# Kernel optimization log

Hardware: AMD Instinct MI355X
Metric: run time of the kernel (lower is better)

The kernel has to match this reference:

```python
import jax, jax.numpy as jnp
import numpy as np


def setup_inputs() -> dict:
    key = jax.random.key(0)
    ks = jax.random.split(key, 7)
    N = 262144
    Ka, La = 8, 8
    Kb, Lb, Mb = 8, 8, 4
    Kc, Lc, Mc = 8, 8, 4
    return {
        "x": jax.random.normal(ks[0], (N, 2), dtype=jnp.float32),
        "a_real": 0.001 * jax.random.normal(ks[1], (Ka, La), dtype=jnp.float32),
        "a_imag": 0.001 * jax.random.normal(ks[2], (Ka, La), dtype=jnp.float32),
        "b_real": 0.001 * jax.random.normal(ks[3], (Kb, Lb, Mb), dtype=jnp.float32),
        "b_imag": 0.001 * jax.random.normal(ks[4], (Kb, Lb, Mb), dtype=jnp.float32),
        "c_real": 0.001 * jax.random.normal(ks[5], (Kc, Lc, Mc), dtype=jnp.float32),
        "c_imag": 0.001 * jax.random.normal(ks[6], (Kc, Lc, Mc), dtype=jnp.float32),
    }


def _gmp(x, a_real, a_imag, b_real, b_imag, c_real, c_imag):
    # x: (N,2) real I/Q -> complex signal (iq_handler equivalent)
    xc = (x[:, 0] + 1j * x[:, 1]).astype(jnp.complex64)
    a = (a_real + 1j * a_imag).astype(jnp.complex64)   # (Ka,La)
    b = (b_real + 1j * b_imag).astype(jnp.complex64)   # (Kb,Lb,Mb)
    c = (c_real + 1j * c_imag).astype(jnp.complex64)   # (Kc,Lc,Mc)
    N = xc.shape[0]
    Ka, La = a.shape
    Kb, Lb, Mb = b.shape
    Kc, Lc, Mc = c.shape
    n = jnp.arange(N)

    # ---- aligned term (a): delayed taps, power series in |x[n-l]| ----
    idx_La = jnp.clip(n[None, :] - jnp.arange(La)[:, None], 0, N - 1)   # (La,N)
    x_La = xc[idx_La]                                                   # (La,N)
    pow_a = jnp.abs(x_La)[..., None] ** jnp.arange(Ka, dtype=jnp.float32)  # (La,N,Ka)
    term_a = jnp.einsum('kl,ln,lnk->n', a, x_La, pow_a)

    # ---- lagging cross-term (b): envelope delayed by extra m >= 0 ----
    idx_Lb = jnp.clip(n[None, :] - jnp.arange(Lb)[:, None], 0, N - 1)   # (Lb,N)
    x_Lb = xc[idx_Lb]                                                   # (Lb,N)
    idx_Mb = jnp.clip(n[None, None, :] - jnp.arange(Lb)[:, None, None]
                      - jnp.arange(Mb)[None, :, None], 0, N - 1)        # (Lb,Mb,N)
    x_Mb = xc[idx_Mb]                                                   # (Lb,Mb,N)
    pow_b = jnp.abs(x_Mb)[..., None] ** jnp.arange(Kb, dtype=jnp.float32)  # (Lb,Mb,N,Kb)
    term_b = jnp.einsum('klm,ln,lmnk->n', b, x_Lb, pow_b)

    # ---- leading cross-term (c): envelope advanced by m >= 0 ----
    idx_Lc = jnp.clip(n[None, :] - jnp.arange(Lc)[:, None], 0, N - 1)   # (Lc,N)
    x_Lc = xc[idx_Lc]                                                   # (Lc,N)
    idx_Mc = jnp.clip(n[None, None, :] - jnp.arange(Lc)[:, None, None]
                      + jnp.arange(Mc)[None, :, None], 0, N - 1)        # (Lc,Mc,N)
    x_Mc = xc[idx_Mc]                                                   # (Lc,Mc,N)
    pow_c = jnp.abs(x_Mc)[..., None] ** jnp.arange(Kc, dtype=jnp.float32)  # (Lc,Mc,N,Kc)
    term_c = jnp.einsum('klm,ln,lmnk->n', c, x_Lc, pow_c)

    y = term_a + term_b + term_c                                        # (N,) complex
    return jnp.stack([y.real, y.imag], axis=-1)                         # back to I/Q (N,2)


def reference(x, a_real, a_imag, b_real, b_imag, c_real, c_imag):
    return _gmp(x, a_real, a_imag, b_real, b_imag, c_real, c_imag)
```

## Files before the change

### kernel.cpp

```cpp
#include <hip/hip_runtime.h>
#include <type_traits>

typedef float v2f __attribute__((ext_vector_type(2)));

constexpr int BLOCK = 512;
constexpr int CHUNKS = 4;
constexpr int SPB = 256;
constexpr int SPBLK = SPB * CHUNKS;
constexpr int HALO_LO = 10;
constexpr int HALO_HI = 3;
constexpr int SIG = SPB + HALO_LO + HALO_HI;
constexpr int PSTRIDE = 128;

template<int I, int N, typename F>
__device__ __forceinline__ void unroll_for(F&& f) {
    if constexpr (I < N) {
        f(std::integral_constant<int, I>{});
        unroll_for<I + 1, N>(static_cast<F&&>(f));
    }
}

__global__ __launch_bounds__(BLOCK, 2) void gmp_kernel(
    const float* __restrict__ x,
    const float* __restrict__ a_re, const float* __restrict__ a_im,
    const float* __restrict__ b_re, const float* __restrict__ b_im,
    const float* __restrict__ c_re, const float* __restrict__ c_im,
    float* __restrict__ out, int N)
{
    __shared__ float sxr[SIG], sxi[SIG], sab[SIG];
    __shared__ __align__(16) float2 part[8][SPB];
    __shared__ __align__(16) float wlds[896];

    const int t = threadIdx.x;
    const int blk0 = blockIdx.x * SPBLK;
    const float2* x2 = (const float2*)x;

    if (t < SIG) {
        int g = blk0 - HALO_LO + t;
        g = max(0, min(N - 1, g));
        float2 v = x2[g];
        sxr[t] = v.x;
        sxi[t] = v.y;
        sab[t] = __builtin_amdgcn_sqrtf(fmaf(v.x, v.x, v.y * v.y));
    }

    if (t < 448) {
        int idx = t;
        int l = idx / 56;
        int rem = idx - l * 56;
        int s = rem >> 3;
        int k = rem & 7;
        int akl = k * 8 + l;
        float re, im;
        if (s == 0) {
            re = a_re[akl] + b_re[akl * 4] + c_re[akl * 4];
            im = a_im[akl] + b_im[akl * 4] + c_im[akl * 4];
        } else if (s <= 3) {
            re = b_re[akl * 4 + s];
            im = b_im[akl * 4 + s];
        } else {
            re = c_re[akl * 4 + (s - 3)];
            im = c_im[akl * 4 + (s - 3)];
        }
        wlds[idx * 2]     = re;
        wlds[idx * 2 + 1] = im;
    }
    __syncthreads();

    const int s2 = t & 63;
    const int wv = __builtin_amdgcn_readfirstlane(t >> 6);
    const float* cw = &wlds[wv * 112];

    v2f wk[7][8];
    unroll_for<0, 7>([&](auto Sc) {
        unroll_for<0, 8>([&](auto K) {
            wk[Sc.value][K.value] =
                *(const v2f*)&cw[Sc.value * 16 + 2 * K.value];
        });
    });

    const int rb0 = 2 * s2 + 7 - wv;
    const int rb1 = rb0 + PSTRIDE;

    for (int c = 0; c < CHUNKS; ++c) {
        const int n0 = blk0 + c * SPB;

        if (c > 0) {
            if (t < SIG) {
                int g = n0 - HALO_LO + t;
                g = max(0, min(N - 1, g));
                float2 v = x2[g];
                sxr[t] = v.x;
                sxi[t] = v.y;
                sab[t] = __builtin_amdgcn_sqrtf(fmaf(v.x, v.x, v.y * v.y));
            }
            __syncthreads();
        }

        float rvA[8], rvB[8];
        unroll_for<0, 8>([&](auto I) {
            rvA[I.value] = sab[rb0 + I.value];
            rvB[I.value] = sab[rb1 + I.value];
        });
        float xArr[2], xAri[2], xBrr[2], xBri[2];
        unroll_for<0, 2>([&](auto Q) {
            xArr[Q.value] = sxr[rb0 + 3 + Q.value];
            xAri[Q.value] = sxi[rb0 + 3 + Q.value];
            xBrr[Q.value] = sxr[rb1 + 3 + Q.value];
            xBri[Q.value] = sxi[rb1 + 3 + Q.value];
        });

        v2f S[4] = {{0.f,0.f},{0.f,0.f},{0.f,0.f},{0.f,0.f}};
        unroll_for<0, 7>([&](auto Sc) {
            constexpr int s = Sc.value;
            constexpr int d3 = (s == 0) ? 3 : ((s <= 3) ? (3 - s) : s);
            const float r0A = rvA[0 + d3];
            const float r1A = rvA[1 + d3];
            const float r0B = rvB[0 + d3];
            const float r1B = rvB[1 + d3];
            v2f acc0 = wk[s][7], acc1 = acc0, acc2 = acc0, acc3 = acc0;
            unroll_for<0, 7>([&](auto Kc) {
                constexpr int k = 6 - Kc.value;
                acc0 = __builtin_elementwise_fma(acc0, (v2f){r0A, r0A}, wk[s][k]);
                acc1 = __builtin_elementwise_fma(acc1, (v2f){r1A, r1A}, wk[s][k]);
                acc2 = __builtin_elementwise_fma(acc2, (v2f){r0B, r0B}, wk[s][k]);
                acc3 = __builtin_elementwise_fma(acc3, (v2f){r1B, r1B}, wk[s][k]);
            });
            S[0] += acc0;
            S[1] += acc1;
            S[2] += acc2;
            S[3] += acc3;
        });

        {
            float pr0 = xArr[0]*S[0].x - xAri[0]*S[0].y;
            float pi0 = xArr[0]*S[0].y + xAri[0]*S[0].x;
            float pr1 = xArr[1]*S[1].x - xAri[1]*S[1].y;
            float pi1 = xArr[1]*S[1].y + xAri[1]*S[1].x;
            *(float4*)&part[wv][2 * s2] = make_float4(pr0, pi0, pr1, pi1);
            float qr0 = xBrr[0]*S[2].x - xBri[0]*S[2].y;
            float qi0 = xBrr[0]*S[2].y + xBri[0]*S[2].x;
            float qr1 = xBrr[1]*S[3].x - xBri[1]*S[3].y;
            float qi1 = xBrr[1]*S[3].y + xBri[1]*S[3].x;
            *(float4*)&part[wv][2 * s2 + PSTRIDE] = make_float4(qr0, qi0, qr1, qi1);
        }
        __syncthreads();

        if (t < SPB) {
            float2 p0 = part[0][t], p1 = part[1][t];
            float2 p2 = part[2][t], p3 = part[3][t];
            float2 p4 = part[4][t], p5 = part[5][t];
            float2 p6 = part[6][t], p7 = part[7][t];
            float2 r;
            r.x = ((p0.x + p1.x) + (p2.x + p3.x)) + ((p4.x + p5.x) + (p6.x + p7.x));
            r.y = ((p0.y + p1.y) + (p2.y + p3.y)) + ((p4.y + p5.y) + (p6.y + p7.y));
            const int n = n0 + t;
            if (n < N) ((float2*)out)[n] = r;
        }
    }
}

extern "C" void kernel_launch(void* const* d_in, const int* in_sizes, int n_in,
                              void* d_out, int out_size, void* d_ws, size_t ws_size,
                              hipStream_t stream) {
    const float* x    = (const float*)d_in[0];
    const float* a_re = (const float*)d_in[1];
    const float* a_im = (const float*)d_in[2];
    const float* b_re = (const float*)d_in[3];
    const float* b_im = (const float*)d_in[4];
    const float* c_re = (const float*)d_in[5];
    const float* c_im = (const float*)d_in[6];
    float* out = (float*)d_out;

    int N = in_sizes[0] / 2;
    int grid = (N + SPBLK - 1) / SPBLK;
    gmp_kernel<<<grid, BLOCK, 0, stream>>>(x, a_re, a_im, b_re, b_im,
                                           c_re, c_im, out, N);
}
```

Baseline: 12.80 us.

## Double-buffer signal and partial-sum LDS to prefetch next chunk during compute

Shared signal and partial-sum buffers are doubled so the next chunk's global load is issued before the current chunk's compute and written to the alternate buffer afterward. This removes one __syncthreads per chunk and hides global load latency behind the FMA work. The launch-bounds occupancy hint of 2 blocks per CU is also dropped, which may change register allocation and occupancy. LDS use roughly doubles for those buffers.

```diff
diff --git a/kernel.cpp b/kernel.cpp
--- a/kernel.cpp
+++ b/kernel.cpp
@@ -20,15 +20,15 @@
     }
 }
 
-__global__ __launch_bounds__(BLOCK, 2) void gmp_kernel(
+__global__ __launch_bounds__(BLOCK) void gmp_kernel(
     const float* __restrict__ x,
     const float* __restrict__ a_re, const float* __restrict__ a_im,
     const float* __restrict__ b_re, const float* __restrict__ b_im,
     const float* __restrict__ c_re, const float* __restrict__ c_im,
     float* __restrict__ out, int N)
 {
-    __shared__ float sxr[SIG], sxi[SIG], sab[SIG];
-    __shared__ __align__(16) float2 part[8][SPB];
+    __shared__ float sxr[2][SIG], sxi[2][SIG], sab[2][SIG];
+    __shared__ __align__(16) float2 part[2][8][SPB];
     __shared__ __align__(16) float wlds[896];
 
     const int t = threadIdx.x;
@@ -39,9 +39,9 @@
         int g = blk0 - HALO_LO + t;
         g = max(0, min(N - 1, g));
         float2 v = x2[g];
-        sxr[t] = v.x;
-        sxi[t] = v.y;
-        sab[t] = __builtin_amdgcn_sqrtf(fmaf(v.x, v.x, v.y * v.y));
+        sxr[0][t] = v.x;
+        sxi[0][t] = v.y;
+        sab[0][t] = __builtin_amdgcn_sqrtf(fmaf(v.x, v.x, v.y * v.y));
     }
 
     if (t < 448) {
@@ -83,31 +83,28 @@
     const int rb1 = rb0 + PSTRIDE;
 
     for (int c = 0; c < CHUNKS; ++c) {
+        const int cur = c & 1;
         const int n0 = blk0 + c * SPB;
 
-        if (c > 0) {
-            if (t < SIG) {
-                int g = n0 - HALO_LO + t;
-                g = max(0, min(N - 1, g));
-                float2 v = x2[g];
-                sxr[t] = v.x;
-                sxi[t] = v.y;
-                sab[t] = __builtin_amdgcn_sqrtf(fmaf(v.x, v.x, v.y * v.y));
-            }
-            __syncthreads();
+        float2 nv;
+        const bool do_stage = (c + 1 < CHUNKS) && (t < SIG);
+        if (do_stage) {
+            int g = n0 + SPB - HALO_LO + t;
+            g = max(0, min(N - 1, g));
+            nv = x2[g];
         }
 
         float rvA[8], rvB[8];
         unroll_for<0, 8>([&](auto I) {
-            rvA[I.value] = sab[rb0 + I.value];
-            rvB[I.value] = sab[rb1 + I.value];
+            rvA[I.value] = sab[cur][rb0 + I.value];
+            rvB[I.value] = sab[cur][rb1 + I.value];
         });
         float xArr[2], xAri[2], xBrr[2], xBri[2];
         unroll_for<0, 2>([&](auto Q) {
-            xArr[Q.value] = sxr[rb0 + 3 + Q.value];
-            xAri[Q.value] = sxi[rb0 + 3 + Q.value];
-            xBrr[Q.value] = sxr[rb1 + 3 + Q.value];
-            xBri[Q.value] = sxi[rb1 + 3 + Q.value];
+            xArr[Q.value] = sxr[cur][rb0 + 3 + Q.value];
+            xAri[Q.value] = sxi[cur][rb0 + 3 + Q.value];
+            xBrr[Q.value] = sxr[cur][rb1 + 3 + Q.value];
+            xBri[Q.value] = sxi[cur][rb1 + 3 + Q.value];
         });
 
         v2f S[4] = {{0.f,0.f},{0.f,0.f},{0.f,0.f},{0.f,0.f}};
@@ -137,20 +134,27 @@
             float pi0 = xArr[0]*S[0].y + xAri[0]*S[0].x;
             float pr1 = xArr[1]*S[1].x - xAri[1]*S[1].y;
             float pi1 = xArr[1]*S[1].y + xAri[1]*S[1].x;
-            *(float4*)&part[wv][2 * s2] = make_float4(pr0, pi0, pr1, pi1);
+            *(float4*)&part[cur][wv][2 * s2] = make_float4(pr0, pi0, pr1, pi1);
             float qr0 = xBrr[0]*S[2].x - xBri[0]*S[2].y;
             float qi0 = xBrr[0]*S[2].y + xBri[0]*S[2].x;
             float qr1 = xBrr[1]*S[3].x - xBri[1]*S[3].y;
             float qi1 = xBrr[1]*S[3].y + xBri[1]*S[3].x;
-            *(float4*)&part[wv][2 * s2 + PSTRIDE] = make_float4(qr0, qi0, qr1, qi1);
+            *(float4*)&part[cur][wv][2 * s2 + PSTRIDE] = make_float4(qr0, qi0, qr1, qi1);
         }
+
+        if (do_stage) {
+            sxr[cur ^ 1][t] = nv.x;
+            sxi[cur ^ 1][t] = nv.y;
+            sab[cur ^ 1][t] = __builtin_amdgcn_sqrtf(fmaf(nv.x, nv.x, nv.y * nv.y));
+        }
+
         __syncthreads();
 
         if (t < SPB) {
-            float2 p0 = part[0][t], p1 = part[1][t];
-            float2 p2 = part[2][t], p3 = part[3][t];
-            float2 p4 = part[4][t], p5 = part[5][t];
-            float2 p6 = part[6][t], p7 = part[7][t];
+            float2 p0 = part[cur][0][t], p1 = part[cur][1][t];
+            float2 p2 = part[cur][2][t], p3 = part[cur][3][t];
+            float2 p4 = part[cur][4][t], p5 = part[cur][5][t];
+            float2 p6 = part[cur][6][t], p7 = part[cur][7][t];
             float2 r;
             r.x = ((p0.x + p1.x) + (p2.x + p3.x)) + ((p4.x + p5.x) + (p6.x + p7.x));
             r.y = ((p0.y + p1.y) + (p2.y + p3.y)) + ((p4.y + p5.y) + (p6.y + p7.y));
```

Measured after the change: 12.82 us. Within noise of the previous version (+0.2%).
